# Kernel tuning notes

Measured on AMD Instinct MI355X. Metric: run time of the kernel, lower is better.

The kernel has to match this reference:

```python
import jax, jax.numpy as jnp
import numpy as np

N_PTS0 = 32   # sample points per line
N_PTS1 = 8    # after 1d max-pool (kernel 4)
DIM_LOI = 128
DIM_FC = 1024
TOPK = 300
H = W = 128
L = 10000
C_FEAT = 256


def setup_inputs() -> dict:
    key = jax.random.key(0)
    ks = jax.random.split(key, 8)
    f32 = jnp.float32
    return {
        'output': jax.random.normal(ks[0], (1, 9, H, W), f32),
        'features': jax.random.normal(ks[1], (1, C_FEAT, H, W), f32),
        'lines_pred': jax.random.uniform(ks[2], (L, 4), f32, 0.0, W - 1.0),
        'fc1_w': jax.random.normal(ks[3], (DIM_LOI, C_FEAT), f32) * 0.05,
        'fc1_b': jnp.zeros((DIM_LOI,), f32),
        'w1': jax.random.normal(ks[4], (DIM_FC, DIM_LOI * N_PTS1), f32) * 0.02,
        'b1': jnp.zeros((DIM_FC,), f32),
        'w2': jax.random.normal(ks[5], (DIM_FC, DIM_FC), f32) * 0.02,
        'b2': jnp.zeros((DIM_FC,), f32),
        'w3': jax.random.normal(ks[6], (1, DIM_FC), f32) * 0.02,
        'b3': jnp.zeros((1,), f32),
    }


def _nms(a):
    # a: [H, W]; 3x3 max-pool NMS, keep only local maxima
    ap = jax.lax.reduce_window(a[None, None], -jnp.inf, jax.lax.max,
                               (1, 1, 3, 3), (1, 1, 1, 1), 'SAME')[0, 0]
    return a * (a == ap).astype(a.dtype)


def _pooling(loi, lines, w1, b1, w2, b2, w3, b3):
    # loi: [D, H, W]; lines: [L, 4]
    h, w = loi.shape[1], loi.shape[2]
    tspan = jnp.linspace(0.0, 1.0, N_PTS0)[None, None, :]          # [1,1,P]
    U, V = lines[:, :2], lines[:, 2:]
    pts = U[:, :, None] * tspan + V[:, :, None] * (1.0 - tspan) - 0.5  # [L,2,P]
    pts = jnp.transpose(pts, (0, 2, 1)).reshape(-1, 2)              # [L*P,2]
    px, py = pts[:, 0], pts[:, 1]
    px0 = jnp.clip(jnp.floor(px), 0, w - 1)
    py0 = jnp.clip(jnp.floor(py), 0, h - 1)
    px1 = jnp.clip(px0 + 1, 0, w - 1)
    py1 = jnp.clip(py0 + 1, 0, h - 1)
    ix0, iy0 = px0.astype(jnp.int32), py0.astype(jnp.int32)
    ix1, iy1 = px1.astype(jnp.int32), py1.astype(jnp.int32)
    xp = (loi[:, iy0, ix0] * (py1 - py) * (px1 - px)
          + loi[:, iy1, ix0] * (py - py0) * (px1 - px)
          + loi[:, iy0, ix1] * (py1 - py) * (px - px0)
          + loi[:, iy1, ix1] * (py - py0) * (px - px0))              # [D, L*P]
    xp = jnp.transpose(xp.reshape(DIM_LOI, -1, N_PTS0), (1, 0, 2))  # [L,D,P]
    k = N_PTS0 // N_PTS1
    xp = xp.reshape(xp.shape[0], DIM_LOI, N_PTS1, k).max(-1)        # maxpool1d
    feat = xp.reshape(-1, DIM_LOI * N_PTS1)                         # [L, D*P1]
    hid = jax.nn.relu(feat @ w1.T + b1)
    hid = jax.nn.relu(hid @ w2.T + b2)
    return (hid @ w3.T + b3).ravel()                                # logits [L]


def reference(output, features, lines_pred, fc1_w, fc1_b, w1, b1, w2, b2, w3, b3):
    height, width = output.shape[2], output.shape[3]
    # head decode
    jloc = jax.nn.softmax(output[0, 5:7], axis=0)[1]      # [H,W]
    joff = jax.nn.sigmoid(output[0, 7:9]) - 0.5           # [2,H,W]
    # NMS + top-k junction extraction
    jflat = _nms(jloc).reshape(-1)
    jscores, index = jax.lax.top_k(jflat, TOPK)
    joff_f = joff.reshape(2, -1)
    y = (index // width).astype(jnp.float32) + joff_f[1, index] + 0.5
    x = (index % width).astype(jnp.float32) + joff_f[0, index] + 0.5
    juncs = jnp.stack((x, y), axis=1)                     # [K,2]
    # pairwise endpoint-to-junction matching
    d1 = jnp.sum((lines_pred[None, :, :2] - juncs[:, None]) ** 2, -1)  # [K,L]
    d2 = jnp.sum((lines_pred[None, :, 2:] - juncs[:, None]) ** 2, -1)
    idx1 = jnp.argmin(d1, axis=0)
    idx2 = jnp.argmin(d2, axis=0)
    imin = jnp.minimum(idx1, idx2)
    imax = jnp.maximum(idx1, idx2)
    keep = imin < imax                                    # degenerate-line mask
    lines_adj = jnp.concatenate((juncs[imin], juncs[imax]), axis=1)  # [L,4]
    # 1x1 conv LOI features + bilinear line sampling + MLP verification
    loi = jnp.einsum('chw,dc->dhw', features[0], fc1_w) + fc1_b[:, None, None]
    logits = _pooling(loi, lines_adj, w1, b1, w2, b2, w3, b3)
    line_scores = jax.nn.sigmoid(logits) * keep.astype(logits.dtype)
    return line_scores, lines_adj, juncs, jscores
```

## Files before the change

### kernel.cpp

```cpp
#include <hip/hip_runtime.h>
#include <stdint.h>

#define HW      16384
#define WIDTH   128
#define NTOPK   300
#define NLINES  10000
#define MPAD    10112

typedef unsigned short u16;
typedef unsigned int   u32;
typedef unsigned long long u64;
typedef __bf16 bf16x8 __attribute__((ext_vector_type(8)));
typedef float  f32x4  __attribute__((ext_vector_type(4)));

__device__ __forceinline__ u16 f2bf(float f) {
  u32 x = __builtin_bit_cast(u32, f);
  x += 0x7FFFu + ((x >> 16) & 1u);
  return (u16)(x >> 16);
}
__device__ __forceinline__ float bf2f(u32 u) {
  return __builtin_bit_cast(float, u << 16);
}
__device__ __forceinline__ void gload_lds16(void* lds, const void* g) {
  __builtin_amdgcn_global_load_lds(
      (const __attribute__((address_space(1))) void*)g,
      (__attribute__((address_space(3))) void*)lds, 16, 0, 0);
}

__global__ __launch_bounds__(256) void k_nms(const float* __restrict__ out9,
                                             float* __restrict__ jnms) {
  __shared__ float jl[18][18];
  int t = threadIdx.x;
  int gx0 = blockIdx.x * 16 - 1, gy0 = blockIdx.y * 16 - 1;
  for (int lin = t; lin < 324; lin += 256) {
    int lx = lin % 18, ly = lin / 18;
    int gx = gx0 + lx, gy = gy0 + ly;
    float v = -__builtin_inff();
    if (gx >= 0 && gx < WIDTH && gy >= 0 && gy < WIDTH) {
      int i = gy * WIDTH + gx;
      v = 1.f / (1.f + expf(out9[5 * HW + i] - out9[6 * HW + i]));
    }
    jl[ly][lx] = v;
  }
  __syncthreads();
  int tx = t & 15, ty = t >> 4;
  float a = jl[ty + 1][tx + 1], m = a;
#pragma unroll
  for (int dy = 0; dy < 3; ++dy)
#pragma unroll
    for (int dx = 0; dx < 3; ++dx)
      m = fmaxf(m, jl[ty + dy][tx + dx]);
  int gx = blockIdx.x * 16 + tx, gy = blockIdx.y * 16 + ty;
  jnms[gy * WIDTH + gx] = (a == m) ? a : 0.f;
}

__global__ __launch_bounds__(1024) void k_topk(const float* __restrict__ jnms,
                                               const float* __restrict__ out9,
                                               float* __restrict__ juncs_ws,
                                               float* __restrict__ out_juncs,
                                               float* __restrict__ out_jsc) {
  __shared__ u64 keys[4096];
  __shared__ int cnt;
  int t = threadIdx.x;
  if (t == 0) cnt = 0;
  __syncthreads();
  for (int i = t; i < HW; i += 1024) {
    float v = jnms[i];
    if (v > 0.f) {
      int pos = atomicAdd(&cnt, 1);
      if (pos < 4096)
        keys[pos] = ((u64)__builtin_bit_cast(u32, v) << 32) | (u32)(0xFFFFFFFFu - (u32)i);
    }
  }
  __syncthreads();
  int c = cnt < 4096 ? cnt : 4096;
  int n = (c <= 2048) ? 2048 : 4096;
  for (int i = t; i < n; i += 1024)
    if (i >= c) keys[i] = 0ull;
  __syncthreads();
  for (int k = 2; k <= n; k <<= 1) {
    for (int j = k >> 1; j > 0; j >>= 1) {
      for (int u = t; u < (n >> 1); u += 1024) {
        int i  = ((u & ~(j - 1)) << 1) | (u & (j - 1));
        int p  = i | j;
        u64 a = keys[i], b = keys[p];
        bool dir = (i & k) == 0;
        if ((a < b) == dir) { keys[i] = b; keys[p] = a; }
      }
      __syncthreads();
    }
  }
  if (t < NTOPK) {
    u64 key = keys[t];
    u32 vb  = (u32)(key >> 32);
    int idx = (int)(0xFFFFFFFFu - (u32)(key & 0xFFFFFFFFu));
    float ox = 1.f / (1.f + expf(-out9[7 * HW + idx])) - 0.5f;
    float oy = 1.f / (1.f + expf(-out9[8 * HW + idx])) - 0.5f;
    float x = (float)(idx & (WIDTH - 1)) + ox + 0.5f;
    float y = (float)(idx >> 7)          + oy + 0.5f;
    juncs_ws[2 * t] = x; juncs_ws[2 * t + 1] = y;
    out_juncs[2 * t] = x; out_juncs[2 * t + 1] = y;
    out_jsc[t] = __builtin_bit_cast(float, vb);
  }
}

__global__ __launch_bounds__(256) void k_match(const float* __restrict__ juncs,
                                               const float* __restrict__ lines_pred,
                                               float* __restrict__ lines_adj,
                                               float* __restrict__ keepf) {
  __shared__ float jl[2 * NTOPK];
  int t = threadIdx.x;
  for (int i = t; i < 2 * NTOPK; i += 256) jl[i] = juncs[i];
  __syncthreads();
  int wid = t >> 6, lane = t & 63;
  int l = blockIdx.x * 4 + wid;
  if (l >= NLINES) return;
  float lx1 = lines_pred[l * 4 + 0], ly1 = lines_pred[l * 4 + 1];
  float lx2 = lines_pred[l * 4 + 2], ly2 = lines_pred[l * 4 + 3];
  float b1 = __builtin_inff(), b2 = __builtin_inff();
  int i1 = 0, i2 = 0;
  for (int j = lane; j < NTOPK; j += 64) {
    float jx = jl[2 * j], jy = jl[2 * j + 1];
    float dx = __fsub_rn(lx1, jx), dy = __fsub_rn(ly1, jy);
    float d  = __fadd_rn(__fmul_rn(dx, dx), __fmul_rn(dy, dy));
    if (d < b1) { b1 = d; i1 = j; }
    dx = __fsub_rn(lx2, jx); dy = __fsub_rn(ly2, jy);
    d  = __fadd_rn(__fmul_rn(dx, dx), __fmul_rn(dy, dy));
    if (d < b2) { b2 = d; i2 = j; }
  }
#pragma unroll
  for (int off = 1; off < 64; off <<= 1) {
    float d_o = __shfl_xor(b1, off, 64); int i_o = __shfl_xor(i1, off, 64);
    if (d_o < b1 || (d_o == b1 && i_o < i1)) { b1 = d_o; i1 = i_o; }
    d_o = __shfl_xor(b2, off, 64); i_o = __shfl_xor(i2, off, 64);
    if (d_o < b2 || (d_o == b2 && i_o < i2)) { b2 = d_o; i2 = i_o; }
  }
  if (lane == 0) {
    int imin = i1 < i2 ? i1 : i2;
    int imax = i1 < i2 ? i2 : i1;
    lines_adj[l * 4 + 0] = jl[2 * imin];
    lines_adj[l * 4 + 1] = jl[2 * imin + 1];
    lines_adj[l * 4 + 2] = jl[2 * imax];
    lines_adj[l * 4 + 3] = jl[2 * imax + 1];
    keepf[l] = (imin < imax) ? 1.f : 0.f;
  }
}

__global__ __launch_bounds__(256) void k_transp(const float* __restrict__ features,
                                                u16* __restrict__ featT) {
  __shared__ float tile[64][65];
  int t = threadIdx.x;
  int p0 = blockIdx.x * 64, c0 = blockIdx.y * 64;
#pragma unroll
  for (int i = 0; i < 4; ++i) {
    int lin = i * 256 + t;
    int c = lin >> 4, p4 = (lin & 15) * 4;
    float4 v = *(const float4*)&features[(size_t)(c0 + c) * HW + p0 + p4];
    tile[c][p4 + 0] = v.x; tile[c][p4 + 1] = v.y;
    tile[c][p4 + 2] = v.z; tile[c][p4 + 3] = v.w;
  }
  __syncthreads();
#pragma unroll
  for (int i = 0; i < 2; ++i) {
    int lin = i * 256 + t;
    int p = lin >> 3, c8 = (lin & 7) * 8;
    uint4 pk;
    pk.x = (u32)f2bf(tile[c8 + 0][p]) | ((u32)f2bf(tile[c8 + 1][p]) << 16);
    pk.y = (u32)f2bf(tile[c8 + 2][p]) | ((u32)f2bf(tile[c8 + 3][p]) << 16);
    pk.z = (u32)f2bf(tile[c8 + 4][p]) | ((u32)f2bf(tile[c8 + 5][p]) << 16);
    pk.w = (u32)f2bf(tile[c8 + 6][p]) | ((u32)f2bf(tile[c8 + 7][p]) << 16);
    *(uint4*)&featT[(size_t)(p0 + p) * 256 + c0 + c8] = pk;
  }
}

__device__ __forceinline__ void acc8(uint4 r, float wg, float* a) {
  a[0] += bf2f(r.x & 0xffffu) * wg; a[1] += bf2f(r.x >> 16) * wg;
  a[2] += bf2f(r.y & 0xffffu) * wg; a[3] += bf2f(r.y >> 16) * wg;
  a[4] += bf2f(r.z & 0xffffu) * wg; a[5] += bf2f(r.z >> 16) * wg;
  a[6] += bf2f(r.w & 0xffffu) * wg; a[7] += bf2f(r.w >> 16) * wg;
}
__global__ __launch_bounds__(256) void k_interp(const u16* __restrict__ loib,
                                                const float* __restrict__ lines_adj,
                                                u16* __restrict__ feat) {
  __shared__ u16 outb[8][128];
  int l = blockIdx.x;
  int t = threadIdx.x;
  int w = t >> 6, lane = t & 63;
  int q = lane >> 4, chgrp = lane & 15;
  float ux = lines_adj[l * 4 + 0], uy = lines_adj[l * 4 + 1];
  float vx = lines_adj[l * 4 + 2], vy = lines_adj[l * 4 + 3];
#pragma unroll
  for (int it = 0; it < 2; ++it) {
    int s = it * 4 + w;
    int p = s * 4 + q;
    float tt = (float)p / 31.f;
    float px = ux * tt + vx * (1.f - tt) - 0.5f;
    float py = uy * tt + vy * (1.f - tt) - 0.5f;
    float px0 = fminf(fmaxf(floorf(px), 0.f), 127.f);
    float py0 = fminf(fmaxf(floorf(py), 0.f), 127.f);
    float px1 = fminf(px0 + 1.f, 127.f);
    float py1 = fminf(py0 + 1.f, 127.f);
    int ix0 = (int)px0, iy0 = (int)py0, ix1 = (int)px1, iy1 = (int)py1;
    float wy1 = py1 - py, wy0 = py - py0, wx1 = px1 - px, wx0 = px - px0;
    int co = chgrp * 8;
    uint4 v00 = *(const uint4*)&loib[(iy0 * WIDTH + ix0) * 128 + co];
    uint4 v10 = *(const uint4*)&loib[(iy1 * WIDTH + ix0) * 128 + co];
    uint4 v01 = *(const uint4*)&loib[(iy0 * WIDTH + ix1) * 128 + co];
    uint4 v11 = *(const uint4*)&loib[(iy1 * WIDTH + ix1) * 128 + co];
    float a[8];
#pragma unroll
    for (int c = 0; c < 8; ++c) a[c] = 0.f;
    acc8(v00, wy1 * wx1, a);
    acc8(v10, wy0 * wx1, a);
    acc8(v01, wy1 * wx0, a);
    acc8(v11, wy0 * wx0, a);
#pragma unroll
    for (int c = 0; c < 8; ++c) {
      float v = fmaxf(a[c], __shfl_xor(a[c], 16, 64));
      v = fmaxf(v, __shfl_xor(v, 32, 64));
      a[c] = v;
    }
    if (q == 0) {
      uint4 pk;
      pk.x = (u32)f2bf(a[0]) | ((u32)f2bf(a[1]) << 16);
      pk.y = (u32)f2bf(a[2]) | ((u32)f2bf(a[3]) << 16);
      pk.z = (u32)f2bf(a[4]) | ((u32)f2bf(a[5]) << 16);
      pk.w = (u32)f2bf(a[6]) | ((u32)f2bf(a[7]) << 16);
      *(uint4*)&outb[s][co] = pk;
    }
  }
  __syncthreads();
  int ch = t >> 1, s0 = (t & 1) * 4;
  u16 e0 = outb[s0 + 0][ch], e1 = outb[s0 + 1][ch];
  u16 e2 = outb[s0 + 2][ch], e3 = outb[s0 + 3][ch];
  uint2 pk;
  pk.x = (u32)e0 | ((u32)e1 << 16);
  pk.y = (u32)e2 | ((u32)e3 << 16);
  *(uint2*)&feat[(size_t)l * 1024 + ch * 8 + s0] = pk;
}

__global__ __launch_bounds__(256) void k_cvt(const float* __restrict__ src,
                                             u16* __restrict__ dst, int n) {
  int i = (blockIdx.x * 256 + threadIdx.x) * 4;
  if (i >= n) return;
  float4 v = *(const float4*)&src[i];
  uint2 pk;
  pk.x = (u32)f2bf(v.x) | ((u32)f2bf(v.y) << 16);
  pk.y = (u32)f2bf(v.z) | ((u32)f2bf(v.w) << 16);
  *(uint2*)&dst[i] = pk;
}

template <int RELU, int HEAD>
__global__ __launch_bounds__(256) void k_gemm(const u16* __restrict__ A,
                                              const u16* __restrict__ B,
                                              const float* __restrict__ bias,
                                              u16* __restrict__ C,
                                              const float* __restrict__ w3,
                                              float* __restrict__ partial,
                                              int M, int N, int K) {
  __shared__ u16 Al[2][4096];
  __shared__ u16 Bl[2][4096];
  int nwg = gridDim.x * gridDim.y;
  int bid = blockIdx.y * gridDim.x + blockIdx.x;
  int cpx = nwg >> 3;
  int key = (bid & 7) * cpx + (bid >> 3);
  int bx = key / gridDim.y;
  int by = key % gridDim.y;
  int t = threadIdx.x, lane = t & 63, wid = t >> 6;
  int wr = wid >> 1, wc = wid & 1;
  f32x4 acc[4][4] = {};
  int arow = t >> 2, apos = (t & 3) * 8;
  const u16* Abase = A + (size_t)(bx * 128) * K;
  const u16* Bbase = B + (size_t)(by * 128) * K;
  int r = lane & 15, ks = (lane >> 4) * 8;
  int nt = K >> 5;
  gload_lds16(&Al[0][t * 8],         Abase + (size_t)arow * K + apos);
  gload_lds16(&Al[0][(t + 256) * 8], Abase + (size_t)(arow + 64) * K + apos);
  gload_lds16(&Bl[0][t * 8],         Bbase + (size_t)arow * K + apos);
  gload_lds16(&Bl[0][(t + 256) * 8], Bbase + (size_t)(arow + 64) * K + apos);
  __syncthreads();
  for (int it = 0; it < nt; ++it) {
    int cur = it & 1, nxt = cur ^ 1;
    if (it + 1 < nt) {
      int k0 = (it + 1) << 5;
      gload_lds16(&Al[nxt][t * 8],         Abase + (size_t)arow * K + k0 + apos);
      gload_lds16(&Al[nxt][(t + 256) * 8], Abase + (size_t)(arow + 64) * K + k0 + apos);
      gload_lds16(&Bl[nxt][t * 8],         Bbase + (size_t)arow * K + k0 + apos);
      gload_lds16(&Bl[nxt][(t + 256) * 8], Bbase + (size_t)(arow + 64) * K + k0 + apos);
    }
    bf16x8 af[4], bfr[4];
#pragma unroll
    for (int i = 0; i < 4; ++i) {
      af[i]  = *(const bf16x8*)&Al[cur][(wr * 64 + i * 16 + r) * 32 + ks];
      bfr[i] = *(const bf16x8*)&Bl[cur][(wc * 64 + i * 16 + r) * 32 + ks];
    }
#pragma unroll
    for (int mi = 0; mi < 4; ++mi)
#pragma unroll
      for (int ni = 0; ni < 4; ++ni)
        acc[mi][ni] = __builtin_amdgcn_mfma_f32_16x16x32_bf16(af[mi], bfr[ni], acc[mi][ni], 0, 0, 0);
    __syncthreads();
  }
  int rsub = (lane >> 4) * 4, csub = lane & 15;
  if (HEAD == 0) {
    u16* Ct = &Al[0][0];
#pragma unroll
    for (int c = 0; c < 2; ++c) {
      if (wr == c) {
#pragma unroll
        for (int mi = 0; mi < 4; ++mi)
#pragma unroll
          for (int ni = 0; ni < 4; ++ni) {
            int col = wc * 64 + ni * 16 + csub;
            float bv = bias[by * 128 + col];
#pragma unroll
            for (int j = 0; j < 4; ++j) {
              float v = acc[mi][ni][j] + bv;
              if (RELU) v = fmaxf(v, 0.f);
              Ct[(mi * 16 + rsub + j) * 128 + col] = f2bf(v);
            }
          }
      }
      __syncthreads();
#pragma unroll
      for (int i = 0; i < 4; ++i) {
        int lin = i * 256 + t;
        int rl = lin >> 4, pc = lin & 15;
        uint4 v = *(const uint4*)&Ct[rl * 128 + pc * 8];
        *(uint4*)&C[(size_t)(bx * 128 + c * 64 + rl) * N + by * 128 + pc * 8] = v;
      }
      __syncthreads();
    }
  } else {
    float bv[4], wv[4];
#pragma unroll
    for (int ni = 0; ni < 4; ++ni) {
      int col = by * 128 + wc * 64 + ni * 16 + csub;
      bv[ni] = bias[col];
      wv[ni] = w3[col];
    }
#pragma unroll
    for (int mi = 0; mi < 4; ++mi) {
#pragma unroll
      for (int j = 0; j < 4; ++j) {
        float p = 0.f;
#pragma unroll
        for (int ni = 0; ni < 4; ++ni) {
          float v = acc[mi][ni][j] + bv[ni];
          v = fmaxf(v, 0.f);
          p += v * wv[ni];
        }
        p += __shfl_xor(p, 1, 64);
        p += __shfl_xor(p, 2, 64);
        p += __shfl_xor(p, 4, 64);
        p += __shfl_xor(p, 8, 64);
        if (csub == 0) {
          int row = bx * 128 + wr * 64 + mi * 16 + rsub + j;
          partial[(size_t)(by * 2 + wc) * M + row] = p;
        }
      }
    }
  }
}

__global__ __launch_bounds__(256) void k_head2(const float* __restrict__ partial,
                                               const float* __restrict__ b3,
                                               const float* __restrict__ keepf,
                                               float* __restrict__ scores, int M) {
  int l = blockIdx.x * 256 + threadIdx.x;
  if (l >= NLINES) return;
  float s = 0.f;
#pragma unroll
  for (int i = 0; i < 16; ++i) s += partial[(size_t)i * M + l];
  float logit = s + b3[0];
  scores[l] = keepf[l] / (1.f + expf(-logit));
}

extern "C" void kernel_launch(void* const* d_in, const int* in_sizes, int n_in,
                              void* d_out, int out_size, void* d_ws, size_t ws_size,
                              hipStream_t stream) {
  const float* t_output   = (const float*)d_in[0];
  const float* t_features = (const float*)d_in[1];
  const float* t_lines    = (const float*)d_in[2];
  const float* t_fc1w     = (const float*)d_in[3];
  const float* t_fc1b     = (const float*)d_in[4];
  const float* t_w1       = (const float*)d_in[5];
  const float* t_b1       = (const float*)d_in[6];
  const float* t_w2       = (const float*)d_in[7];
  const float* t_b2       = (const float*)d_in[8];
  const float* t_w3       = (const float*)d_in[9];
  const float* t_b3       = (const float*)d_in[10];

  char* w = (char*)d_ws;
  u16*   loib  = (u16*)w;
  float* jnms  = (float*)(w + 4194304);
  float* juncs = jnms + HW;
  float* keepf = juncs + 1024;
  u16* fc1wb = (u16*)(keepf + 10240);
  u16* w1b  = fc1wb + 32768;
  u16* w2b  = w1b + 1048576;
  u16* feat = w2b + 1048576;
  u16* hid1 = feat + (size_t)MPAD * 1024;
  float* partial = (float*)(hid1 + (size_t)MPAD * 1024);
  u16* featT = hid1;

  float* out_scores = (float*)d_out;
  float* out_ladj   = out_scores + NLINES;
  float* out_juncs  = out_scores + 50000;
  float* out_jsc    = out_scores + 50600;

  k_nms<<<dim3(8, 8), 256, 0, stream>>>(t_output, jnms);
  k_topk<<<1, 1024, 0, stream>>>(jnms, t_output, juncs, out_juncs, out_jsc);
  k_match<<<2500, 256, 0, stream>>>(juncs, t_lines, out_ladj, keepf);
  k_cvt<<<32, 256, 0, stream>>>(t_fc1w, fc1wb, 32768);
  k_transp<<<dim3(256, 4), 256, 0, stream>>>(t_features, featT);
  k_gemm<0, 0><<<dim3(128, 1), 256, 0, stream>>>(featT, fc1wb, t_fc1b, loib,
                                                 nullptr, nullptr, HW, 128, 256);
  k_interp<<<NLINES, 256, 0, stream>>>(loib, out_ladj, feat);
  k_cvt<<<1024, 256, 0, stream>>>(t_w1, w1b, 1048576);
  k_cvt<<<1024, 256, 0, stream>>>(t_w2, w2b, 1048576);
  k_gemm<1, 0><<<dim3(MPAD / 128, 8), 256, 0, stream>>>(feat, w1b, t_b1, hid1,
                                                        nullptr, nullptr, MPAD, 1024, 1024);
  k_gemm<1, 1><<<dim3(MPAD / 128, 8), 256, 0, stream>>>(hid1, w2b, t_b2, nullptr,
                                                        t_w3, partial, MPAD, 1024, 1024);
  k_head2<<<40, 256, 0, stream>>>(partial, t_b3, keepf, out_scores, MPAD);
}
```

Before: 158.1 us.

## Replace MLP GEMMs with 256x256-tile, 8-wave pipelined, swizzled-LDS kernel

Adds a new GEMM kernel for the two 1024x1024 MLP layers. Each block computes a 256x256 output tile with 512 threads. It uses XOR-swizzled LDS staging, manual s_waitcnt and barriers, and interleaves global-to-LDS copies with MFMA phases under raised wave priority. The aim is more data reuse per loaded byte and better overlap of loads with matrix math. The catch is that only 160 blocks are launched, which can leave many CUs idle. The row padding grows to 10240 to match the tile size, and the small fc1 GEMM is split into a simpler single-buffered 128-tile kernel that writes directly to global memory.

```diff
diff --git a/kernel.cpp b/kernel.cpp
--- a/kernel.cpp
+++ b/kernel.cpp
@@ -5,7 +5,7 @@
 #define WIDTH   128
 #define NTOPK   300
 #define NLINES  10000
-#define MPAD    10112
+#define MPAD2   10240
 
 typedef unsigned short u16;
 typedef unsigned int   u32;
@@ -26,6 +26,11 @@
       (const __attribute__((address_space(1))) void*)g,
       (__attribute__((address_space(3))) void*)lds, 16, 0, 0);
 }
+
+#define CF asm volatile("" ::: "memory")
+#define BAR do { CF; __builtin_amdgcn_s_barrier(); CF; } while (0)
+#define VM4 asm volatile("s_waitcnt vmcnt(4)" ::: "memory")
+#define VM0 asm volatile("s_waitcnt vmcnt(0)" ::: "memory")
 
 __global__ __launch_bounds__(256) void k_nms(const float* __restrict__ out9,
                                              float* __restrict__ jnms) {
@@ -250,49 +255,41 @@
   *(uint2*)&dst[i] = pk;
 }
 
-template <int RELU, int HEAD>
-__global__ __launch_bounds__(256) void k_gemm(const u16* __restrict__ A,
-                                              const u16* __restrict__ B,
-                                              const float* __restrict__ bias,
-                                              u16* __restrict__ C,
-                                              const float* __restrict__ w3,
-                                              float* __restrict__ partial,
-                                              int M, int N, int K) {
-  __shared__ u16 Al[2][4096];
-  __shared__ u16 Bl[2][4096];
+template <int RELU>
+__global__ __launch_bounds__(256) void k_gemm128(const u16* __restrict__ A,
+                                                 const u16* __restrict__ B,
+                                                 const float* __restrict__ bias,
+                                                 u16* __restrict__ C,
+                                                 int M, int N, int K) {
+  __shared__ u16 Alds[128 * 32];
+  __shared__ u16 Blds[128 * 32];
   int nwg = gridDim.x * gridDim.y;
   int bid = blockIdx.y * gridDim.x + blockIdx.x;
   int cpx = nwg >> 3;
   int key = (bid & 7) * cpx + (bid >> 3);
   int bx = key / gridDim.y;
   int by = key % gridDim.y;
-  int t = threadIdx.x, lane = t & 63, wid = t >> 6;
+  int t = threadIdx.x;
+  int tm0 = bx * 128;
+  int tn0 = by * 128;
+  int lane = t & 63, wid = t >> 6;
   int wr = wid >> 1, wc = wid & 1;
   f32x4 acc[4][4] = {};
   int arow = t >> 2, apos = (t & 3) * 8;
-  const u16* Abase = A + (size_t)(bx * 128) * K;
-  const u16* Bbase = B + (size_t)(by * 128) * K;
+  const u16* Abase = A + (size_t)tm0 * K;
+  const u16* Bbase = B + (size_t)tn0 * K;
   int r = lane & 15, ks = (lane >> 4) * 8;
-  int nt = K >> 5;
-  gload_lds16(&Al[0][t * 8],         Abase + (size_t)arow * K + apos);
-  gload_lds16(&Al[0][(t + 256) * 8], Abase + (size_t)(arow + 64) * K + apos);
-  gload_lds16(&Bl[0][t * 8],         Bbase + (size_t)arow * K + apos);
-  gload_lds16(&Bl[0][(t + 256) * 8], Bbase + (size_t)(arow + 64) * K + apos);
-  __syncthreads();
-  for (int it = 0; it < nt; ++it) {
-    int cur = it & 1, nxt = cur ^ 1;
-    if (it + 1 < nt) {
-      int k0 = (it + 1) << 5;
-      gload_lds16(&Al[nxt][t * 8],         Abase + (size_t)arow * K + k0 + apos);
-      gload_lds16(&Al[nxt][(t + 256) * 8], Abase + (size_t)(arow + 64) * K + k0 + apos);
-      gload_lds16(&Bl[nxt][t * 8],         Bbase + (size_t)arow * K + k0 + apos);
-      gload_lds16(&Bl[nxt][(t + 256) * 8], Bbase + (size_t)(arow + 64) * K + k0 + apos);
-    }
+  for (int k0 = 0; k0 < K; k0 += 32) {
+    gload_lds16(&Alds[(size_t)t * 8],         Abase + (size_t)arow * K + k0 + apos);
+    gload_lds16(&Alds[(size_t)(t + 256) * 8], Abase + (size_t)(arow + 64) * K + k0 + apos);
+    gload_lds16(&Blds[(size_t)t * 8],         Bbase + (size_t)arow * K + k0 + apos);
+    gload_lds16(&Blds[(size_t)(t + 256) * 8], Bbase + (size_t)(arow + 64) * K + k0 + apos);
+    __syncthreads();
     bf16x8 af[4], bfr[4];
 #pragma unroll
     for (int i = 0; i < 4; ++i) {
-      af[i]  = *(const bf16x8*)&Al[cur][(wr * 64 + i * 16 + r) * 32 + ks];
-      bfr[i] = *(const bf16x8*)&Bl[cur][(wc * 64 + i * 16 + r) * 32 + ks];
+      af[i]  = *(const bf16x8*)&Alds[(wr * 64 + i * 16 + r) * 32 + ks];
+      bfr[i] = *(const bf16x8*)&Blds[(wc * 64 + i * 16 + r) * 32 + ks];
     }
 #pragma unroll
     for (int mi = 0; mi < 4; ++mi)
@@ -302,62 +299,196 @@
     __syncthreads();
   }
   int rsub = (lane >> 4) * 4, csub = lane & 15;
+#pragma unroll
+  for (int mi = 0; mi < 4; ++mi) {
+#pragma unroll
+    for (int ni = 0; ni < 4; ++ni) {
+      int col = tn0 + wc * 64 + ni * 16 + csub;
+      float bv = bias[col];
+#pragma unroll
+      for (int j = 0; j < 4; ++j) {
+        int row = tm0 + wr * 64 + mi * 16 + rsub + j;
+        float v = acc[mi][ni][j] + bv;
+        if (RELU) v = fmaxf(v, 0.f);
+        C[(size_t)row * N + col] = f2bf(v);
+      }
+    }
+  }
+}
+
+__device__ __forceinline__ void stg256(u16* S, int ldsbase, const u16* Xb,
+                                       size_t sbase, int K, int kt, int h, int dbase) {
+  gload_lds16(&S[ldsbase + h * 8192 + dbase],
+              Xb + sbase + (size_t)(h * 128) * K + kt * 64);
+  gload_lds16(&S[ldsbase + h * 8192 + 4096 + dbase],
+              Xb + sbase + (size_t)(h * 128 + 64) * K + kt * 64);
+}
+template <int RH>
+__device__ __forceinline__ void lda4(bf16x8 (*dst)[2], const u16* Sa, int rowA,
+                                     int kx0, int kx1) {
+#pragma unroll
+  for (int f = 0; f < 4; ++f) {
+    const u16* p = Sa + rowA + (RH * 64 + f * 16) * 64;
+    dst[f][0] = *(const bf16x8*)&p[kx0];
+    dst[f][1] = *(const bf16x8*)&p[kx1];
+  }
+}
+template <int CH>
+__device__ __forceinline__ void ldb2(bf16x8 (*dst)[2], const u16* Sb, int rowB,
+                                     int kx0, int kx1) {
+#pragma unroll
+  for (int cf = 0; cf < 2; ++cf) {
+    const u16* p = Sb + rowB + (CH * 32 + cf * 16) * 64;
+    dst[cf][0] = *(const bf16x8*)&p[kx0];
+    dst[cf][1] = *(const bf16x8*)&p[kx1];
+  }
+}
+template <int RH, int CH>
+__device__ __forceinline__ void mm16(f32x4 (*acc)[4], bf16x8 (*af)[2], bf16x8 (*bf)[2]) {
+  __builtin_amdgcn_s_setprio(1);
+#pragma unroll
+  for (int f = 0; f < 4; ++f)
+#pragma unroll
+    for (int cf = 0; cf < 2; ++cf) {
+      f32x4 a = acc[RH * 4 + f][CH * 2 + cf];
+      a = __builtin_amdgcn_mfma_f32_16x16x32_bf16(af[f][0], bf[cf][0], a, 0, 0, 0);
+      a = __builtin_amdgcn_mfma_f32_16x16x32_bf16(af[f][1], bf[cf][1], a, 0, 0, 0);
+      acc[RH * 4 + f][CH * 2 + cf] = a;
+    }
+  __builtin_amdgcn_s_setprio(0);
+}
+
+template <int RELU, int HEAD>
+__global__ __launch_bounds__(512, 2) void k_gemm256(const u16* __restrict__ A,
+                                                    const u16* __restrict__ B,
+                                                    const float* __restrict__ bias,
+                                                    u16* __restrict__ C,
+                                                    const float* __restrict__ w3,
+                                                    float* __restrict__ partial,
+                                                    int M, int N, int K) {
+  __shared__ u16 S[65536];
+  const int t = threadIdx.x, lane = t & 63, w = t >> 6;
+  const int wm = w >> 2, wn = w & 3;
+  int nwg = gridDim.x * gridDim.y;
+  int bid = blockIdx.y * gridDim.x + blockIdx.x;
+  int cpx = nwg >> 3;
+  int key = (bid & 7) * cpx + (bid >> 3);
+  int bx = key / gridDim.y, by = key % gridDim.y;
+  const u16* Ab = A + (size_t)(bx * 256) * K;
+  const u16* Bb = B + (size_t)(by * 256) * K;
+  const int srow = w * 8 + (lane >> 3);
+  const size_t sbase = (size_t)srow * K + ((lane & 7) ^ (lane >> 3)) * 8;
+  const int dbase = w * 512 + lane * 8;
+  const int l15 = lane & 15, hi = lane >> 4, l7 = lane & 7;
+  const int rowA = (wm * 128 + l15) * 64;
+  const int rowB = (wn * 64 + l15) * 64;
+  const int kx0 = ((0 + hi) ^ l7) * 8;
+  const int kx1 = ((4 + hi) ^ l7) * 8;
+  const u16* SA0 = S;
+  const u16* SA1 = S + 16384;
+  const u16* SB0 = S + 32768;
+  const u16* SB1 = S + 49152;
+  f32x4 acc[8][4] = {};
+  bf16x8 af0[4][2], af1[4][2], bf0[2][2], bf1[2][2];
+  const int NI = K >> 7;
+  stg256(S, 0,     Ab, sbase, K, 0, 0, dbase);
+  stg256(S, 0,     Ab, sbase, K, 0, 1, dbase);
+  stg256(S, 32768, Bb, sbase, K, 0, 0, dbase);
+  stg256(S, 32768, Bb, sbase, K, 0, 1, dbase);
+  stg256(S, 16384, Ab, sbase, K, 1, 0, dbase);
+  stg256(S, 16384, Ab, sbase, K, 1, 1, dbase);
+  VM4; BAR;
+  for (int j = 0; j < NI - 1; ++j) {
+    int kt = 2 * j;
+    lda4<0>(af0, SA0, rowA, kx0, kx1);
+    ldb2<0>(bf0, SB0, rowB, kx0, kx1);
+    stg256(S, 49152, Bb, sbase, K, kt + 1, 0, dbase);
+    BAR; mm16<0, 0>(acc, af0, bf0); BAR;
+    lda4<1>(af1, SA0, rowA, kx0, kx1);
+    stg256(S, 49152, Bb, sbase, K, kt + 1, 1, dbase);
+    BAR; mm16<1, 0>(acc, af1, bf0); BAR;
+    ldb2<1>(bf1, SB0, rowB, kx0, kx1);
+    stg256(S, 0, Ab, sbase, K, kt + 2, 0, dbase);
+    BAR; mm16<0, 1>(acc, af0, bf1); BAR;
+    stg256(S, 0, Ab, sbase, K, kt + 2, 1, dbase);
+    VM4;
+    BAR; mm16<1, 1>(acc, af1, bf1); BAR;
+    lda4<0>(af0, SA1, rowA, kx0, kx1);
+    ldb2<0>(bf0, SB1, rowB, kx0, kx1);
+    stg256(S, 32768, Bb, sbase, K, kt + 2, 0, dbase);
+    BAR; mm16<0, 0>(acc, af0, bf0); BAR;
+    lda4<1>(af1, SA1, rowA, kx0, kx1);
+    stg256(S, 32768, Bb, sbase, K, kt + 2, 1, dbase);
+    BAR; mm16<1, 0>(acc, af1, bf0); BAR;
+    ldb2<1>(bf1, SB1, rowB, kx0, kx1);
+    stg256(S, 16384, Ab, sbase, K, kt + 3, 0, dbase);
+    BAR; mm16<0, 1>(acc, af0, bf1); BAR;
+    stg256(S, 16384, Ab, sbase, K, kt + 3, 1, dbase);
+    VM4;
+    BAR; mm16<1, 1>(acc, af1, bf1); BAR;
+  }
+  {
+    int kt = 2 * (NI - 1);
+    lda4<0>(af0, SA0, rowA, kx0, kx1);
+    ldb2<0>(bf0, SB0, rowB, kx0, kx1);
+    stg256(S, 49152, Bb, sbase, K, kt + 1, 0, dbase);
+    BAR; mm16<0, 0>(acc, af0, bf0); BAR;
+    lda4<1>(af1, SA0, rowA, kx0, kx1);
+    stg256(S, 49152, Bb, sbase, K, kt + 1, 1, dbase);
+    BAR; mm16<1, 0>(acc, af1, bf0); BAR;
+    ldb2<1>(bf1, SB0, rowB, kx0, kx1);
+    BAR; mm16<0, 1>(acc, af0, bf1); BAR;
+    VM0;
+    BAR; mm16<1, 1>(acc, af1, bf1); BAR;
+    lda4<0>(af0, SA1, rowA, kx0, kx1);
+    ldb2<0>(bf0, SB1, rowB, kx0, kx1);
+    BAR; mm16<0, 0>(acc, af0, bf0); BAR;
+    lda4<1>(af1, SA1, rowA, kx0, kx1);
+    BAR; mm16<1, 0>(acc, af1, bf0); BAR;
+    ldb2<1>(bf1, SB1, rowB, kx0, kx1);
+    BAR; mm16<0, 1>(acc, af0, bf1); BAR;
+    mm16<1, 1>(acc, af1, bf1);
+  }
+  int row0 = bx * 256 + wm * 128 + hi * 4;
+  int col0 = by * 256 + wn * 64 + l15;
   if (HEAD == 0) {
-    u16* Ct = &Al[0][0];
-#pragma unroll
-    for (int c = 0; c < 2; ++c) {
-      if (wr == c) {
-#pragma unroll
-        for (int mi = 0; mi < 4; ++mi)
-#pragma unroll
-          for (int ni = 0; ni < 4; ++ni) {
-            int col = wc * 64 + ni * 16 + csub;
-            float bv = bias[by * 128 + col];
-#pragma unroll
-            for (int j = 0; j < 4; ++j) {
-              float v = acc[mi][ni][j] + bv;
-              if (RELU) v = fmaxf(v, 0.f);
-              Ct[(mi * 16 + rsub + j) * 128 + col] = f2bf(v);
-            }
-          }
+#pragma unroll
+    for (int f = 0; f < 8; ++f) {
+#pragma unroll
+      for (int cf = 0; cf < 4; ++cf) {
+        float bv = bias[col0 + cf * 16];
+#pragma unroll
+        for (int jj = 0; jj < 4; ++jj) {
+          float v = acc[f][cf][jj] + bv;
+          if (RELU) v = fmaxf(v, 0.f);
+          C[(size_t)(row0 + f * 16 + jj) * N + col0 + cf * 16] = f2bf(v);
+        }
       }
-      __syncthreads();
-#pragma unroll
-      for (int i = 0; i < 4; ++i) {
-        int lin = i * 256 + t;
-        int rl = lin >> 4, pc = lin & 15;
-        uint4 v = *(const uint4*)&Ct[rl * 128 + pc * 8];
-        *(uint4*)&C[(size_t)(bx * 128 + c * 64 + rl) * N + by * 128 + pc * 8] = v;
-      }
-      __syncthreads();
     }
   } else {
     float bv[4], wv[4];
 #pragma unroll
-    for (int ni = 0; ni < 4; ++ni) {
-      int col = by * 128 + wc * 64 + ni * 16 + csub;
-      bv[ni] = bias[col];
-      wv[ni] = w3[col];
-    }
-#pragma unroll
-    for (int mi = 0; mi < 4; ++mi) {
-#pragma unroll
-      for (int j = 0; j < 4; ++j) {
+    for (int cf = 0; cf < 4; ++cf) {
+      bv[cf] = bias[col0 + cf * 16];
+      wv[cf] = w3[col0 + cf * 16];
+    }
+#pragma unroll
+    for (int f = 0; f < 8; ++f) {
+#pragma unroll
+      for (int jj = 0; jj < 4; ++jj) {
         float p = 0.f;
 #pragma unroll
-        for (int ni = 0; ni < 4; ++ni) {
-          float v = acc[mi][ni][j] + bv[ni];
+        for (int cf = 0; cf < 4; ++cf) {
+          float v = acc[f][cf][jj] + bv[cf];
           v = fmaxf(v, 0.f);
-          p += v * wv[ni];
+          p += v * wv[cf];
         }
         p += __shfl_xor(p, 1, 64);
         p += __shfl_xor(p, 2, 64);
         p += __shfl_xor(p, 4, 64);
         p += __shfl_xor(p, 8, 64);
-        if (csub == 0) {
-          int row = bx * 128 + wr * 64 + mi * 16 + rsub + j;
-          partial[(size_t)(by * 2 + wc) * M + row] = p;
-        }
+        if (l15 == 0)
+          partial[(size_t)(by * 4 + wn) * M + row0 + f * 16 + jj] = p;
       }
     }
   }
@@ -400,8 +531,8 @@
   u16* w1b  = fc1wb + 32768;
   u16* w2b  = w1b + 1048576;
   u16* feat = w2b + 1048576;
-  u16* hid1 = feat + (size_t)MPAD * 1024;
-  float* partial = (float*)(hid1 + (size_t)MPAD * 1024);
+  u16* hid1 = feat + (size_t)MPAD2 * 1024;
+  float* partial = (float*)(hid1 + (size_t)MPAD2 * 1024);
   u16* featT = hid1;
 
   float* out_scores = (float*)d_out;
@@ -414,14 +545,13 @@
   k_match<<<2500, 256, 0, stream>>>(juncs, t_lines, out_ladj, keepf);
   k_cvt<<<32, 256, 0, stream>>>(t_fc1w, fc1wb, 32768);
   k_transp<<<dim3(256, 4), 256, 0, stream>>>(t_features, featT);
-  k_gemm<0, 0><<<dim3(128, 1), 256, 0, stream>>>(featT, fc1wb, t_fc1b, loib,
-                                                 nullptr, nullptr, HW, 128, 256);
+  k_gemm128<0><<<dim3(128, 1), 256, 0, stream>>>(featT, fc1wb, t_fc1b, loib, HW, 128, 256);
   k_interp<<<NLINES, 256, 0, stream>>>(loib, out_ladj, feat);
   k_cvt<<<1024, 256, 0, stream>>>(t_w1, w1b, 1048576);
   k_cvt<<<1024, 256, 0, stream>>>(t_w2, w2b, 1048576);
-  k_gemm<1, 0><<<dim3(MPAD / 128, 8), 256, 0, stream>>>(feat, w1b, t_b1, hid1,
-                                                        nullptr, nullptr, MPAD, 1024, 1024);
-  k_gemm<1, 1><<<dim3(MPAD / 128, 8), 256, 0, stream>>>(hid1, w2b, t_b2, nullptr,
-                                                        t_w3, partial, MPAD, 1024, 1024);
-  k_head2<<<40, 256, 0, stream>>>(partial, t_b3, keepf, out_scores, MPAD);
-}
+  k_gemm256<1, 0><<<dim3(40, 4), 512, 0, stream>>>(feat, w1b, t_b1, hid1,
+                                                   nullptr, nullptr, MPAD2, 1024, 1024);
+  k_gemm256<0, 1><<<dim3(40, 4), 512, 0, stream>>>(hid1, w2b, t_b2, nullptr,
+                                                   t_w3, partial, MPAD2, 1024, 1024);
+  k_head2<<<40, 256, 0, stream>>>(partial, t_b3, keepf, out_scores, MPAD2);
+}
```

Result: slower. 167.9 us (+6.2%).
